# Kernel optimization log

Measured on AMD Instinct MI355X. Metric: run time of the kernel, lower is better.

## Reference

```python
import jax, jax.numpy as jnp
import numpy as np

N = 50000
E = 800000
NFEAT, NHID, NCLASS = 128, 64, 16


def _spmm(row, col, w, x):
    # out[i] = sum_{e: row[e]==i} w[e] * x[col[e]]  -- sparse adj @ x
    return jax.ops.segment_sum(x[col] * w[:, None], row, num_segments=N)


def _gcn_layer(x, row, col, w, W, b):
    return _spmm(row, col, w, x @ W) + b


def setup_inputs() -> dict:
    key = jax.random.key(0)
    ks = jax.random.split(key, 16)
    glorot = lambda k, fi, fo: jax.random.uniform(k, (fi, fo), jnp.float32, -1.0, 1.0) / jnp.sqrt(fi)
    inp = {
        "x": jax.random.normal(ks[0], (N, NFEAT), jnp.float32),
        "edge_row": jax.random.randint(ks[1], (E,), 0, N, jnp.int32),
        "edge_col": jax.random.randint(ks[2], (E,), 0, N, jnp.int32),
        "edge_weight": jax.random.uniform(ks[3], (E,), jnp.float32),
        "W1": glorot(ks[4], NFEAT, NHID), "b1": jnp.zeros((NHID,), jnp.float32),
        "W2": glorot(ks[5], NHID, NHID), "b2": jnp.zeros((NHID,), jnp.float32),
        "W3": glorot(ks[6], NHID, NHID), "b3": jnp.zeros((NHID,), jnp.float32),
        "W4": glorot(ks[7], NHID, NHID), "b4": jnp.zeros((NHID,), jnp.float32),
        "W5": glorot(ks[8], NHID, NCLASS), "b5": jnp.zeros((NCLASS,), jnp.float32),
    }
    return inp


def reference(x, edge_row, edge_col, edge_weight, W1, b1, W2, b2, W3, b3, W4, b4, W5, b5):
    # Inference mode: dropout is identity.
    e1 = _gcn_layer(x, edge_row, edge_col, edge_weight, W1, b1)
    h = jax.nn.relu(e1)
    e2 = _gcn_layer(h, edge_row, edge_col, edge_weight, W2, b2)
    h = jax.nn.relu(e2)
    e3 = _gcn_layer(h, edge_row, edge_col, edge_weight, W3, b3)
    h = jax.nn.relu(e3)
    e4 = _gcn_layer(h, edge_row, edge_col, edge_weight, W4, b4)
    h = jax.nn.relu(e4)
    e5 = _gcn_layer(h, edge_row, edge_col, edge_weight, W5, b5)
    return (jax.nn.log_softmax(e5, axis=1), e1, e2, e3, e4, e5)
```

## Files before the change

kernel.cpp:

```cpp
#include <hip/hip_runtime.h>
#include <math.h>

#define NN 50000
#define NE 800000
#define NFEAT 128
#define NHID 64
#define NCLASS 16
#define NB_SCAN ((NN + 255) / 256)
#define SGRP 4
#define ROWS_PER_SGRP ((NN + SGRP - 1) / SGRP)
#define SCHUNKS 392
#define EMAX 1024
#define EMAX4 512
#define NTILE8 (NN / 8)
#define HG_GEMM 2048

__device__ inline unsigned short f2bf(float f) {
    unsigned u = __builtin_bit_cast(unsigned, f);
    u += 0x7fffu + ((u >> 16) & 1u);
    return (unsigned short)(u >> 16);
}
__device__ inline float bf2f(unsigned short h) {
    return __builtin_bit_cast(float, (unsigned)h << 16);
}
__device__ inline float pk_w(unsigned v) { return bf2f((unsigned short)(v >> 16)); }
__device__ inline int pk_c(unsigned v) { return (int)(v & 0xffffu); }

__global__ __launch_bounds__(256) void hist_gemm_kernel(
    const float* __restrict__ x, const float* __restrict__ W1,
    unsigned short* __restrict__ tmpA,
    const int* __restrict__ erow, const int* __restrict__ ecol,
    const float* __restrict__ ew, int* __restrict__ deg,
    uint2* __restrict__ rr8) {
    __shared__ float xg[8 * 128];
    const int t = threadIdx.x;
    if ((blockIdx.x & 1) == 0) {
        const int j = t & 63;
        const int half = t >> 6;
        const int lr = t >> 5;
        const int lc = (t & 31) * 4;
        for (int tile = blockIdx.x >> 1; tile < NTILE8; tile += HG_GEMM) {
            const int r0 = tile * 8;
            *(float4*)&xg[lr * 128 + lc] = *(const float4*)&x[(size_t)(r0 + lr) * 128 + lc];
            __syncthreads();
            float acc0 = 0.f, acc1 = 0.f;
#pragma unroll 8
            for (int k = 0; k < 128; k++) {
                float w = W1[k * 64 + j];
                acc0 += xg[half * 128 + k] * w;
                acc1 += xg[(half + 4) * 128 + k] * w;
            }
            tmpA[(size_t)(r0 + half) * 64 + j] = f2bf(acc0);
            tmpA[(size_t)(r0 + half + 4) * 64 + j] = f2bf(acc1);
            __syncthreads();
        }
    } else {
        for (int e = (blockIdx.x >> 1) * 256 + t; e < NE; e += HG_GEMM * 256) {
            int r = erow[e];
            int k = atomicAdd(&deg[r], 1);
            uint2 v;
            v.x = ((unsigned)r << 16) | (unsigned)k;
            v.y = ((unsigned)f2bf(ew[e]) << 16) | (unsigned)ecol[e];
            rr8[e] = v;
        }
    }
}

__global__ __launch_bounds__(256) void scan_merged_kernel(const int* __restrict__ deg,
                                                          int* __restrict__ row_ptr, int n) {
    __shared__ int s[256];
    const int t = threadIdx.x;
    const int c = blockIdx.x;

    int part = 0;
    for (int i = t; i < c * 256; i += 256) part += deg[i];
    s[t] = part;
    __syncthreads();
#pragma unroll
    for (int off = 128; off > 0; off >>= 1) {
        if (t < off) s[t] += s[t + off];
        __syncthreads();
    }
    const int blockpre = s[0];
    __syncthreads();

    int i = c * 256 + t;
    int d = (i < n) ? deg[i] : 0;
    s[t] = d;
    __syncthreads();
    for (int off = 1; off < 256; off <<= 1) {
        int u = (t >= off) ? s[t - off] : 0;
        __syncthreads();
        s[t] += u;
        __syncthreads();
    }
    int excl = blockpre + s[t] - d;
    if (i < n) {
        row_ptr[i] = excl;
        if (i == n - 1) row_ptr[n] = excl + d;
    }
}

__global__ __launch_bounds__(256) void scatter_rank8_kernel(const uint2* __restrict__ rr8,
                                                            const int* __restrict__ row_ptr,
                                                            unsigned* __restrict__ pk, int E) {
    const int g = blockIdx.x & (SGRP - 1);
    const int chunk = blockIdx.x / SGRP;
    const int CH = (E + SCHUNKS - 1) / SCHUNKS;
    const int lo = chunk * CH;
    const int hi = (lo + CH < E) ? lo + CH : E;
    const int rlo = g * ROWS_PER_SGRP;
    const int rhi = (rlo + ROWS_PER_SGRP < NN) ? rlo + ROWS_PER_SGRP : NN;
    for (int e = lo + threadIdx.x; e < hi; e += 256) {
        uint2 v = rr8[e];
        int r = (int)(v.x >> 16);
        if (r >= rlo && r < rhi) {
            pk[row_ptr[r] + (int)(v.x & 0xffffu)] = v.y;
        }
    }
}

template <int NOUT>
__global__ __launch_bounds__(256, 8) void spmm64_fused_kernel(
    const unsigned short* __restrict__ gb,
    const int* __restrict__ row_ptr,
    const unsigned* __restrict__ pk,
    const float* __restrict__ bias,
    const float* __restrict__ Wn,
    float* __restrict__ e_out,
    unsigned short* __restrict__ nxt,
    int M) {
    __shared__ float xs[8][64];
    __shared__ unsigned epk[EMAX];
    const int t = threadIdx.x;
    const int lane = t & 63;
    const int rb = t >> 5;
    const int slot = (lane >> 4) & 1;
    const int fl = (lane & 15) * 4;

    const int blk0 = blockIdx.x * 8;
    const int base = row_ptr[blk0];
    const int cnt = row_ptr[blk0 + 8] - base;
    const bool fits = (cnt <= EMAX);
    if (fits) {
        for (int i = t; i < cnt; i += 256) epk[i] = pk[base + i];
    }
    __syncthreads();

    const int r = blk0 + rb;
    float a0 = 0.f, a1 = 0.f, a2 = 0.f, a3 = 0.f;

#define FMA_EDGE(q, g)                                              \
    {                                                               \
        float w_ = pk_w(q);                                         \
        a0 += w_ * bf2f((unsigned short)((g).x & 0xffffu));         \
        a1 += w_ * bf2f((unsigned short)((g).x >> 16));             \
        a2 += w_ * bf2f((unsigned short)((g).y & 0xffffu));         \
        a3 += w_ * bf2f((unsigned short)((g).y >> 16));             \
    }
#define GLD(q) (*(const uint2*)&gb[(size_t)pk_c(q) * 64 + fl])

    if (fits) {
        int le = row_ptr[r] - base;
        const int lend = row_ptr[r + 1] - base;
        for (; le + 16 <= lend; le += 16) {
            unsigned q0 = epk[le + 0 + slot], q1 = epk[le + 2 + slot];
            unsigned q2 = epk[le + 4 + slot], q3 = epk[le + 6 + slot];
            unsigned q4 = epk[le + 8 + slot], q5 = epk[le + 10 + slot];
            unsigned q6 = epk[le + 12 + slot], q7 = epk[le + 14 + slot];
            uint2 g0 = GLD(q0), g1 = GLD(q1), g2 = GLD(q2), g3 = GLD(q3);
            uint2 g4 = GLD(q4), g5 = GLD(q5), g6 = GLD(q6), g7 = GLD(q7);
            FMA_EDGE(q0, g0); FMA_EDGE(q1, g1); FMA_EDGE(q2, g2); FMA_EDGE(q3, g3);
            FMA_EDGE(q4, g4); FMA_EDGE(q5, g5); FMA_EDGE(q6, g6); FMA_EDGE(q7, g7);
        }
        if (le + 8 <= lend) {
            unsigned q0 = epk[le + 0 + slot], q1 = epk[le + 2 + slot];
            unsigned q2 = epk[le + 4 + slot], q3 = epk[le + 6 + slot];
            uint2 g0 = GLD(q0), g1 = GLD(q1), g2 = GLD(q2), g3 = GLD(q3);
            FMA_EDGE(q0, g0); FMA_EDGE(q1, g1); FMA_EDGE(q2, g2); FMA_EDGE(q3, g3);
            le += 8;
        }
        if (le + 4 <= lend) {
            unsigned q0 = epk[le + 0 + slot], q1 = epk[le + 2 + slot];
            uint2 g0 = GLD(q0), g1 = GLD(q1);
            FMA_EDGE(q0, g0); FMA_EDGE(q1, g1);
            le += 4;
        }
        if (le + 2 <= lend) {
            unsigned q = epk[le + slot];
            uint2 g = GLD(q);
            FMA_EDGE(q, g);
            le += 2;
        }
        if (le < lend && slot == 0) {
            unsigned q = epk[le];
            uint2 g = GLD(q);
            FMA_EDGE(q, g);
        }
    } else {
        int e = row_ptr[r];
        const int end = row_ptr[r + 1];
        for (; e + 2 <= end; e += 2) {
            unsigned q = pk[e + slot];
            uint2 g = GLD(q);
            FMA_EDGE(q, g);
        }
        if (e < end && slot == 0) {
            unsigned q = pk[e];
            uint2 g = GLD(q);
            FMA_EDGE(q, g);
        }
    }
#undef GLD

    a0 += __shfl_xor(a0, 16);
    a1 += __shfl_xor(a1, 16);
    a2 += __shfl_xor(a2, 16);
    a3 += __shfl_xor(a3, 16);

    if (slot == 0) {
        float4 b4 = *(const float4*)&bias[fl];
        float4 v;
        v.x = a0 + b4.x;
        v.y = a1 + b4.y;
        v.z = a2 + b4.z;
        v.w = a3 + b4.w;
        *(float4*)&e_out[(size_t)r * 64 + fl] = v;
        xs[rb][fl + 0] = fmaxf(v.x, 0.f);
        xs[rb][fl + 1] = fmaxf(v.y, 0.f);
        xs[rb][fl + 2] = fmaxf(v.z, 0.f);
        xs[rb][fl + 3] = fmaxf(v.w, 0.f);
    }
    __syncthreads();

    if (NOUT == 64) {
        const int rblk = t >> 6;
        const int j = t & 63;
        float acc0 = 0.f, acc1 = 0.f;
#pragma unroll 16
        for (int k = 0; k < 64; k++) {
            float w = Wn[k * 64 + j];
            acc0 += xs[rblk][k] * w;
            acc1 += xs[rblk + 4][k] * w;
        }
        nxt[(size_t)(blk0 + rblk) * 64 + j] = f2bf(acc0);
        nxt[(size_t)(blk0 + rblk + 4) * 64 + j] = f2bf(acc1);
    } else {
        if (t < 8 * NOUT) {
            const int rr = t / NOUT;
            const int j = t % NOUT;
            float acc = 0.f;
#pragma unroll 16
            for (int k = 0; k < 64; k++) acc += xs[rr][k] * Wn[k * NOUT + j];
            nxt[(size_t)(blk0 + rr) * NOUT + j] = f2bf(acc);
        }
    }
}

__global__ __launch_bounds__(256, 8) void spmm16_lsm_kernel(const unsigned short* __restrict__ tmpc,
                                                            const int* __restrict__ row_ptr,
                                                            const unsigned* __restrict__ pk,
                                                            const float* __restrict__ bias,
                                                            float* __restrict__ e5,
                                                            float* __restrict__ out0, int M) {
    __shared__ unsigned epk[EMAX4];
    const int t = threadIdx.x;
    const int lane = t & 63;
    const int wv = t >> 6;
    const int sl = lane >> 2;
    const int fq = (lane & 3) * 4;

    const int blk0 = blockIdx.x * 4;
    const int base = row_ptr[blk0];
    const int cnt = row_ptr[blk0 + 4] - base;
    const bool fits = (cnt <= EMAX4);
    if (fits) {
        for (int i = t; i < cnt; i += 256) epk[i] = pk[base + i];
    }
    __syncthreads();

    const int r = blk0 + wv;
    float a0 = 0.f, a1 = 0.f, a2 = 0.f, a3 = 0.f;
#define FMA_EDGE(q, g)                                      \
    {                                                       \
        float w_ = pk_w(q);                                 \
        a0 += w_ * bf2f((unsigned short)((g).x & 0xffffu)); \
        a1 += w_ * bf2f((unsigned short)((g).x >> 16));     \
        a2 += w_ * bf2f((unsigned short)((g).y & 0xffffu)); \
        a3 += w_ * bf2f((unsigned short)((g).y >> 16));     \
    }
#define GLD16(q) (*(const uint2*)&tmpc[(size_t)pk_c(q) * 16 + fq])
    if (fits) {
        int le = row_ptr[r] - base;
        const int lend = row_ptr[r + 1] - base;
        for (; le + 16 <= lend; le += 16) {
            unsigned q = epk[le + sl];
            uint2 g = GLD16(q);
            FMA_EDGE(q, g);
        }
        int rem = lend - le;
        if (sl < rem) {
            unsigned q = epk[le + sl];
            uint2 g = GLD16(q);
            FMA_EDGE(q, g);
        }
    } else {
        int e = row_ptr[r];
        const int e1 = row_ptr[r + 1];
        for (; e + 16 <= e1; e += 16) {
            unsigned q = pk[e + sl];
            uint2 g = GLD16(q);
            FMA_EDGE(q, g);
        }
        int rem = e1 - e;
        if (sl < rem) {
            unsigned q = pk[e + sl];
            uint2 g = GLD16(q);
            FMA_EDGE(q, g);
        }
    }
#undef GLD16
#undef FMA_EDGE
#pragma unroll
    for (int off = 4; off < 64; off <<= 1) {
        a0 += __shfl_xor(a0, off);
        a1 += __shfl_xor(a1, off);
        a2 += __shfl_xor(a2, off);
        a3 += __shfl_xor(a3, off);
    }
    float4 b4 = *(const float4*)&bias[fq];
    float v0 = a0 + b4.x, v1 = a1 + b4.y, v2 = a2 + b4.z, v3 = a3 + b4.w;

    float m = fmaxf(fmaxf(v0, v1), fmaxf(v2, v3));
    m = fmaxf(m, __shfl_xor(m, 1));
    m = fmaxf(m, __shfl_xor(m, 2));
    float s = expf(v0 - m) + expf(v1 - m) + expf(v2 - m) + expf(v3 - m);
    s += __shfl_xor(s, 1);
    s += __shfl_xor(s, 2);
    float ls = logf(s) + m;
    if (lane < 4) {
        float4 ev = make_float4(v0, v1, v2, v3);
        *(float4*)&e5[(size_t)r * 16 + fq] = ev;
        float4 ov = make_float4(v0 - ls, v1 - ls, v2 - ls, v3 - ls);
        *(float4*)&out0[(size_t)r * 16 + fq] = ov;
    }
}


extern "C" void kernel_launch(void* const* d_in, const int* in_sizes, int n_in,
                              void* d_out, int out_size, void* d_ws, size_t ws_size,
                              hipStream_t stream) {
    const float* x = (const float*)d_in[0];
    const int* erow = (const int*)d_in[1];
    const int* ecol = (const int*)d_in[2];
    const float* ew = (const float*)d_in[3];
    const float* W1 = (const float*)d_in[4];
    const float* b1 = (const float*)d_in[5];
    const float* W2 = (const float*)d_in[6];
    const float* b2 = (const float*)d_in[7];
    const float* W3 = (const float*)d_in[8];
    const float* b3 = (const float*)d_in[9];
    const float* W4 = (const float*)d_in[10];
    const float* b4 = (const float*)d_in[11];
    const float* W5 = (const float*)d_in[12];
    const float* b5 = (const float*)d_in[13];

    float* out0 = (float*)d_out;
    float* e1 = out0 + (size_t)NN * NCLASS;
    float* e2 = e1 + (size_t)NN * NHID;
    float* e3 = e2 + (size_t)NN * NHID;
    float* e4 = e3 + (size_t)NN * NHID;
    float* e5 = e4 + (size_t)NN * NHID;

    char* ws = (char*)d_ws;
    unsigned short* tmpA = (unsigned short*)ws; ws += (size_t)NN * NHID * 2;
    unsigned short* tmpB = (unsigned short*)ws; ws += (size_t)NN * NHID * 2;
    unsigned short* tmpc = (unsigned short*)ws; ws += ((size_t)NN * NCLASS * 2 + 255) / 256 * 256;
    int* deg = (int*)ws;      ws += ((size_t)NN * 4 + 255) / 256 * 256;
    int* row_ptr = (int*)ws;  ws += ((size_t)(NN + 1) * 4 + 255) / 256 * 256;
    uint2* rr8 = (uint2*)ws;  ws += (size_t)NE * 8;
    unsigned* pk = (unsigned*)ws; ws += (size_t)NE * 4;

    hipMemsetAsync(deg, 0, (size_t)NN * 4, stream);

    hist_gemm_kernel<<<2 * HG_GEMM, 256, 0, stream>>>(x, W1, tmpA, erow, ecol, ew, deg, rr8);

    scan_merged_kernel<<<NB_SCAN, 256, 0, stream>>>(deg, row_ptr, NN);

    scatter_rank8_kernel<<<SGRP * SCHUNKS, 256, 0, stream>>>(rr8, row_ptr, pk, NE);

    const int FG = NN / 8;
    spmm64_fused_kernel<64><<<FG, 256, 0, stream>>>(tmpA, row_ptr, pk, b1, W2, e1, tmpB, NN);
    spmm64_fused_kernel<64><<<FG, 256, 0, stream>>>(tmpB, row_ptr, pk, b2, W3, e2, tmpA, NN);
    spmm64_fused_kernel<64><<<FG, 256, 0, stream>>>(tmpA, row_ptr, pk, b3, W4, e3, tmpB, NN);
    spmm64_fused_kernel<16><<<FG, 256, 0, stream>>>(tmpB, row_ptr, pk, b4, W5, e4, tmpc, NN);

    spmm16_lsm_kernel<<<(NN + 3) / 4, 256, 0, stream>>>(tmpc, row_ptr, pk, b5, e5, out0, NN);
}
```

Before: 330.4 us.

## Split fused hist/GEMM kernel into separate histogram and register-tiled GEMM kernels

Replaces the combined kernel, which interleaved the first-layer x@W1 GEMM with the edge histogram/pack work, with two kernels. The histogram kernel becomes a simple one-edge-per-thread launch. The GEMM becomes a dedicated 64-row tiled kernel that stages W1 and a transposed x tile in shared memory and computes a 4x4 register tile per thread, raising data reuse over the old per-8-row naive loop. The cost is an extra launch and losing the overlap between the GEMM and the atomic-heavy histogram, so the two phases now run back to back.

```diff
diff --git a/kernel.cpp b/kernel.cpp
--- a/kernel.cpp
+++ b/kernel.cpp
@@ -7,13 +7,12 @@
 #define NHID 64
 #define NCLASS 16
 #define NB_SCAN ((NN + 255) / 256)
+#define GB ((NN + 63) / 64)
 #define SGRP 4
 #define ROWS_PER_SGRP ((NN + SGRP - 1) / SGRP)
 #define SCHUNKS 392
 #define EMAX 1024
 #define EMAX4 512
-#define NTILE8 (NN / 8)
-#define HG_GEMM 2048
 
 __device__ inline unsigned short f2bf(float f) {
     unsigned u = __builtin_bit_cast(unsigned, f);
@@ -26,43 +25,19 @@
 __device__ inline float pk_w(unsigned v) { return bf2f((unsigned short)(v >> 16)); }
 __device__ inline int pk_c(unsigned v) { return (int)(v & 0xffffu); }
 
-__global__ __launch_bounds__(256) void hist_gemm_kernel(
-    const float* __restrict__ x, const float* __restrict__ W1,
-    unsigned short* __restrict__ tmpA,
-    const int* __restrict__ erow, const int* __restrict__ ecol,
-    const float* __restrict__ ew, int* __restrict__ deg,
-    uint2* __restrict__ rr8) {
-    __shared__ float xg[8 * 128];
-    const int t = threadIdx.x;
-    if ((blockIdx.x & 1) == 0) {
-        const int j = t & 63;
-        const int half = t >> 6;
-        const int lr = t >> 5;
-        const int lc = (t & 31) * 4;
-        for (int tile = blockIdx.x >> 1; tile < NTILE8; tile += HG_GEMM) {
-            const int r0 = tile * 8;
-            *(float4*)&xg[lr * 128 + lc] = *(const float4*)&x[(size_t)(r0 + lr) * 128 + lc];
-            __syncthreads();
-            float acc0 = 0.f, acc1 = 0.f;
-#pragma unroll 8
-            for (int k = 0; k < 128; k++) {
-                float w = W1[k * 64 + j];
-                acc0 += xg[half * 128 + k] * w;
-                acc1 += xg[(half + 4) * 128 + k] * w;
-            }
-            tmpA[(size_t)(r0 + half) * 64 + j] = f2bf(acc0);
-            tmpA[(size_t)(r0 + half + 4) * 64 + j] = f2bf(acc1);
-            __syncthreads();
-        }
-    } else {
-        for (int e = (blockIdx.x >> 1) * 256 + t; e < NE; e += HG_GEMM * 256) {
-            int r = erow[e];
-            int k = atomicAdd(&deg[r], 1);
-            uint2 v;
-            v.x = ((unsigned)r << 16) | (unsigned)k;
-            v.y = ((unsigned)f2bf(ew[e]) << 16) | (unsigned)ecol[e];
-            rr8[e] = v;
-        }
+__global__ __launch_bounds__(256) void hist_pack_kernel(const int* __restrict__ erow,
+                                                        const int* __restrict__ ecol,
+                                                        const float* __restrict__ ew,
+                                                        int* __restrict__ deg,
+                                                        uint2* __restrict__ rr8, int E) {
+    int e = blockIdx.x * 256 + threadIdx.x;
+    if (e < E) {
+        int r = erow[e];
+        int k = atomicAdd(&deg[r], 1);
+        uint2 v;
+        v.x = ((unsigned)r << 16) | (unsigned)k;
+        v.y = ((unsigned)f2bf(ew[e]) << 16) | (unsigned)ecol[e];
+        rr8[e] = v;
     }
 }
 
@@ -116,6 +91,82 @@
         int r = (int)(v.x >> 16);
         if (r >= rlo && r < rhi) {
             pk[row_ptr[r] + (int)(v.x & 0xffffu)] = v.y;
+        }
+    }
+}
+
+template <int K, bool RELU_IN>
+__global__ __launch_bounds__(256) void gemm64_kernel(const float* __restrict__ in,
+                                                     const float* __restrict__ Wg,
+                                                     unsigned short* __restrict__ outb, int M) {
+    constexpr int KC = 64;
+    __shared__ float xs[KC][68];
+    __shared__ float Ws[KC][64];
+    const int t = threadIdx.x;
+    const int tx = t % 16;
+    const int ty = t / 16;
+    const int r0 = blockIdx.x * 64;
+
+    float acc[4][4];
+#pragma unroll
+    for (int i = 0; i < 4; i++)
+#pragma unroll
+        for (int j = 0; j < 4; j++) acc[i][j] = 0.f;
+
+    for (int k0 = 0; k0 < K; k0 += KC) {
+        for (int i = t * 4; i < KC * 64; i += 1024) {
+            *(float4*)&Ws[i / 64][i % 64] = *(const float4*)&Wg[(size_t)k0 * 64 + i];
+        }
+        {
+            const int r = t / 4;
+            const int q = t % 4;
+            const int gr = r0 + r;
+#pragma unroll
+            for (int i = 0; i < 4; i++) {
+                int k = q * 16 + i * 4;
+                float4 v;
+                if (gr < M)
+                    v = *(const float4*)&in[(size_t)gr * K + k0 + k];
+                else
+                    v = make_float4(0.f, 0.f, 0.f, 0.f);
+                if (RELU_IN) {
+                    v.x = fmaxf(v.x, 0.f);
+                    v.y = fmaxf(v.y, 0.f);
+                    v.z = fmaxf(v.z, 0.f);
+                    v.w = fmaxf(v.w, 0.f);
+                }
+                xs[k + 0][r] = v.x;
+                xs[k + 1][r] = v.y;
+                xs[k + 2][r] = v.z;
+                xs[k + 3][r] = v.w;
+            }
+        }
+        __syncthreads();
+#pragma unroll 8
+        for (int k = 0; k < KC; k++) {
+            float4 xv = *(const float4*)&xs[k][ty * 4];
+            float4 wv = *(const float4*)&Ws[k][tx * 4];
+            acc[0][0] += xv.x * wv.x; acc[0][1] += xv.x * wv.y;
+            acc[0][2] += xv.x * wv.z; acc[0][3] += xv.x * wv.w;
+            acc[1][0] += xv.y * wv.x; acc[1][1] += xv.y * wv.y;
+            acc[1][2] += xv.y * wv.z; acc[1][3] += xv.y * wv.w;
+            acc[2][0] += xv.z * wv.x; acc[2][1] += xv.z * wv.y;
+            acc[2][2] += xv.z * wv.z; acc[2][3] += xv.z * wv.w;
+            acc[3][0] += xv.w * wv.x; acc[3][1] += xv.w * wv.y;
+            acc[3][2] += xv.w * wv.z; acc[3][3] += xv.w * wv.w;
+        }
+        __syncthreads();
+    }
+#pragma unroll
+    for (int i = 0; i < 4; i++) {
+        int r = r0 + ty * 4 + i;
+        if (r < M) {
+            ushort4 u;
+            u.x = f2bf(acc[i][0]);
+            u.y = f2bf(acc[i][1]);
+            u.z = f2bf(acc[i][2]);
+            u.w = f2bf(acc[i][3]);
+            *(ushort4*)&outb[(size_t)r * 64 + tx * 4] = u;
         }
     }
 }
@@ -383,11 +434,13 @@
 
     hipMemsetAsync(deg, 0, (size_t)NN * 4, stream);
 
-    hist_gemm_kernel<<<2 * HG_GEMM, 256, 0, stream>>>(x, W1, tmpA, erow, ecol, ew, deg, rr8);
+    hist_pack_kernel<<<(NE + 255) / 256, 256, 0, stream>>>(erow, ecol, ew, deg, rr8, NE);
 
     scan_merged_kernel<<<NB_SCAN, 256, 0, stream>>>(deg, row_ptr, NN);
 
     scatter_rank8_kernel<<<SGRP * SCHUNKS, 256, 0, stream>>>(rr8, row_ptr, pk, NE);
+
+    gemm64_kernel<NFEAT, false><<<GB, 256, 0, stream>>>(x, W1, tmpA, NN);
 
     const int FG = NN / 8;
     spmm64_fused_kernel<64><<<FG, 256, 0, stream>>>(tmpA, row_ptr, pk, b1, W2, e1, tmpB, NN);
```

Result: no change. 330.9 us (+0.2%).
